# Kernel tuning notes

Measured on AMD Instinct MI355X. Metric: run time of the kernel, lower is better.

Reference implementation:

```python
import jax, jax.numpy as jnp
import numpy as np

B, S, D, UNITS = 8, 2048, 512, 512

def setup_inputs() -> dict:
    key = jax.random.key(0)
    k1, k2, k3, k4 = jax.random.split(key, 4)
    scale = 1.0 / np.sqrt(D)
    return {
        "x": jax.random.normal(k1, (B, S, D), dtype=jnp.float32),
        "Wq": jax.random.normal(k2, (D, UNITS), dtype=jnp.float32) * scale,
        "Wk": jax.random.normal(k3, (D, UNITS), dtype=jnp.float32) * scale,
        "Wv": jax.random.normal(k4, (D, UNITS), dtype=jnp.float32) * scale,
    }

def reference(x, Wq, Wk, Wv):
    # Q, K, V: [B, S, units]
    Q = jnp.einsum('bsd,du->bsu', x, Wq)
    Km = jnp.einsum('bsd,du->bsu', x, Wk)
    V = jnp.einsum('bsd,du->bsu', x, Wv)
    d_k = jnp.asarray(Wq.shape[-1], dtype=x.dtype)
    # scores: [B, S, S]
    scores = jnp.einsum('bqu,bku->bqk', Q, Km) / jnp.sqrt(d_k)
    attn = jax.nn.softmax(scores, axis=-1)
    return jnp.einsum('bqk,bku->bqu', attn, V)
```

## Files before the change

kernel.cpp:

```cpp
#include <hip/hip_runtime.h>

typedef __attribute__((ext_vector_type(8))) __bf16 bf16x8;
typedef __attribute__((ext_vector_type(4))) float f32x4;
typedef unsigned short u16;
typedef unsigned int u32;

#define VMCNT(n) asm volatile("s_waitcnt vmcnt(" #n ")" ::: "memory")
#define LGKMCNT0 asm volatile("s_waitcnt lgkmcnt(0)" ::: "memory")

__device__ __forceinline__ u16 f2bf(float f) {
  union { float f; u32 u; } v; v.f = f;
  u32 r = v.u + 0x7FFFu + ((v.u >> 16) & 1u);
  return (u16)(r >> 16);
}
__device__ __forceinline__ float fexp2(float x) {
  float r; asm("v_exp_f32 %0, %1" : "=v"(r) : "v"(x)); return r;
}

__global__ __launch_bounds__(256) void cast_x_kernel(const float* __restrict__ x,
                                                     u16* __restrict__ xb, int n4) {
  int i = blockIdx.x * 256 + threadIdx.x;
  if (i >= n4) return;
  float4 v = reinterpret_cast<const float4*>(x)[i];
  ushort4 o;
  o.x = f2bf(v.x); o.y = f2bf(v.y); o.z = f2bf(v.z); o.w = f2bf(v.w);
  reinterpret_cast<ushort4*>(xb)[i] = o;
}

__global__ __launch_bounds__(1024) void transpose_w_kernel(const float* __restrict__ Wq,
                                                           const float* __restrict__ Wk,
                                                           const float* __restrict__ Wv,
                                                           u16* __restrict__ Wt) {
  const float* src = blockIdx.z == 0 ? Wq : (blockIdx.z == 1 ? Wk : Wv);
  u16* dst = Wt + (size_t)blockIdx.z * 512 * 512;
  __shared__ float tile[32][33];
  int u0 = blockIdx.x * 32, d0 = blockIdx.y * 32;
  tile[threadIdx.y][threadIdx.x] = src[(d0 + threadIdx.y) * 512 + u0 + threadIdx.x];
  __syncthreads();
  dst[(u0 + threadIdx.y) * 512 + d0 + threadIdx.x] = f2bf(tile[threadIdx.x][threadIdx.y]);
}

__global__ __launch_bounds__(256) void qkv_kernel(const u16* __restrict__ Xb,
                                                  const u16* __restrict__ Wt3,
                                                  u16* __restrict__ Q, u16* __restrict__ K,
                                                  u16* __restrict__ Vt2) {
  __shared__ u16 As[3][128 * 32], Bs[3][128 * 32];
  const int bm = blockIdx.y * 128;
  const int bn = blockIdx.x * 128;
  const int z = blockIdx.z;
  const u16* A = Xb + (size_t)bm * 512;
  const u16* Bt = Wt3 + (size_t)z * 512 * 512 + (size_t)bn * 512;

  const int t = threadIdx.x;
  const int lane = t & 63;
  const int w = t >> 6;
  const int wr = w >> 1, wc = w & 1;
  const int la = lane & 15;
  const int q = lane >> 4;
  f32x4 acc[4][4] = {};

  auto stage = [&](int buf, int kt) {
    const int k0 = kt * 32;
#pragma unroll
    for (int it = 0; it < 2; ++it) {
      int c = it * 256 + t, row = c >> 2;
      int col = ((c & 3) ^ ((row >> 1) & 3)) << 3;
      __builtin_amdgcn_global_load_lds(
          (const __attribute__((address_space(1))) void*)(A + (size_t)row * 512 + k0 + col),
          (__attribute__((address_space(3))) void*)(&As[buf][c * 8]), 16, 0, 0);
    }
#pragma unroll
    for (int it = 0; it < 2; ++it) {
      int c = it * 256 + t, row = c >> 2;
      int col = ((c & 3) ^ ((row >> 1) & 3)) << 3;
      __builtin_amdgcn_global_load_lds(
          (const __attribute__((address_space(1))) void*)(Bt + (size_t)row * 512 + k0 + col),
          (__attribute__((address_space(3))) void*)(&Bs[buf][c * 8]), 16, 0, 0);
    }
  };

  auto body = [&](int buf) {
    bf16x8 a[4], b[4];
#pragma unroll
    for (int i = 0; i < 4; ++i) {
      int row = wr * 64 + i * 16 + la;
      a[i] = *reinterpret_cast<const bf16x8*>(&As[buf][row * 32 + ((q ^ ((row >> 1) & 3)) << 3)]);
    }
#pragma unroll
    for (int j = 0; j < 4; ++j) {
      int row = wc * 64 + j * 16 + la;
      b[j] = *reinterpret_cast<const bf16x8*>(&Bs[buf][row * 32 + ((q ^ ((row >> 1) & 3)) << 3)]);
    }
    __builtin_amdgcn_s_setprio(1);
#pragma unroll
    for (int i = 0; i < 4; ++i)
#pragma unroll
      for (int j = 0; j < 4; ++j)
        acc[i][j] = __builtin_amdgcn_mfma_f32_16x16x32_bf16(a[i], b[j], acc[i][j], 0, 0, 0);
    __builtin_amdgcn_s_setprio(0);
  };

  stage(0, 0); stage(1, 1);
  int cb = 0, sb = 2;
  for (int kt = 0; kt < 14; ++kt) {
    VMCNT(4);
    __builtin_amdgcn_s_barrier();
    stage(sb, kt + 2);
    body(cb);
    cb = (cb == 2) ? 0 : cb + 1;
    sb = (sb == 2) ? 0 : sb + 1;
  }
  VMCNT(4); __builtin_amdgcn_s_barrier(); body(2);
  VMCNT(0); __builtin_amdgcn_s_barrier(); body(0);

  const int r0 = q * 4, cn = lane & 15;
  if (z < 2) {
    u16* out = (z == 0) ? Q : K;
#pragma unroll
    for (int i = 0; i < 4; ++i)
#pragma unroll
      for (int j = 0; j < 4; ++j)
#pragma unroll
        for (int r = 0; r < 4; ++r) {
          int m = bm + 64 * wr + 16 * i + r0 + r;
          int n = bn + 64 * wc + 16 * j + cn;
          out[(size_t)m * 512 + n] = f2bf(acc[i][j][r]);
        }
  } else {
#pragma unroll
    for (int i = 0; i < 4; ++i)
#pragma unroll
      for (int j = 0; j < 4; ++j)
#pragma unroll
        for (int r = 0; r < 4; ++r) {
          int m = bm + 64 * wr + 16 * i + r0 + r;
          int u = bn + 64 * wc + 16 * j + cn;
          int b = m >> 11, s = m & 2047;
          Vt2[(((size_t)b * 64 + (s >> 5)) * 512 + u) * 32 + (s & 31)] = f2bf(acc[i][j][r]);
        }
  }
}

__global__ __launch_bounds__(512) void scores8_kernel(const u16* __restrict__ Q,
                                                      const u16* __restrict__ K,
                                                      u16* __restrict__ S2) {
  __shared__ u16 ring[4][2][256 * 32];
  const int bb = blockIdx.x;
  const int bm = blockIdx.y * 256;
  const int bn = blockIdx.z * 256;
  const u16* Aq = Q + (size_t)(bb * 2048 + bm) * 512;
  const u16* Bk = K + (size_t)(bb * 2048 + bn) * 512;

  const int t = threadIdx.x;
  const int lane = t & 63;
  const int wid = t >> 6;
  const int wm = wid >> 2, wn = wid & 3;
  const int la = lane & 15;
  const int q = lane >> 4;

  f32x4 acc[8][4] = {};

  auto stage = [&](int kt) {
    const int r = kt & 3;
    const int koff = kt * 32;
#pragma unroll
    for (int half = 0; half < 2; ++half) {
      int c = half * 512 + t;
      int row = c >> 2;
      int col = ((c & 3) ^ ((row >> 1) & 3)) << 3;
      __builtin_amdgcn_global_load_lds(
          (const __attribute__((address_space(1))) void*)(Aq + (size_t)row * 512 + koff + col),
          (__attribute__((address_space(3))) void*)(&ring[r][0][c * 8]), 16, 0, 0);
      __builtin_amdgcn_global_load_lds(
          (const __attribute__((address_space(1))) void*)(Bk + (size_t)row * 512 + koff + col),
          (__attribute__((address_space(3))) void*)(&ring[r][1][c * 8]), 16, 0, 0);
    }
  };

  auto body = [&](int kt) {
    const int r = kt & 3;
    const u16* At = ring[r][0];
    const u16* Bt = ring[r][1];
    bf16x8 bfr[4], afr[8];
#pragma unroll
    for (int j = 0; j < 4; ++j) {
      int row = wn * 64 + j * 16 + la;
      bfr[j] = *reinterpret_cast<const bf16x8*>(Bt + row * 32 + ((q ^ ((row >> 1) & 3)) << 3));
    }
#pragma unroll
    for (int i = 0; i < 8; ++i) {
      int row = wm * 128 + i * 16 + la;
      afr[i] = *reinterpret_cast<const bf16x8*>(At + row * 32 + ((q ^ ((row >> 1) & 3)) << 3));
    }
    __builtin_amdgcn_s_setprio(1);
#pragma unroll
    for (int i = 0; i < 8; ++i)
#pragma unroll
      for (int j = 0; j < 4; ++j)
        acc[i][j] = __builtin_amdgcn_mfma_f32_16x16x32_bf16(afr[i], bfr[j], acc[i][j], 0, 0, 0);
    __builtin_amdgcn_s_setprio(0);
  };

  stage(0); stage(1); stage(2);
  for (int kt = 0; kt < 13; ++kt) {
    VMCNT(8);
    __builtin_amdgcn_s_barrier();
    stage(kt + 3);
    body(kt);
  }
  VMCNT(8); __builtin_amdgcn_s_barrier(); body(13);
  VMCNT(4); __builtin_amdgcn_s_barrier(); body(14);
  VMCNT(0); __builtin_amdgcn_s_barrier(); body(15);

  const float scale = 0.06375872127f;
  const int r0h = q * 4;
#pragma unroll
  for (int i = 0; i < 8; ++i)
#pragma unroll
    for (int j = 0; j < 4; ++j) {
      int n = bn + wn * 64 + j * 16;
      int kt_j = n >> 5;
      int ke_j = (n & 31) + la;
      u16* dst = S2 + ((size_t)(bb * 64 + kt_j) * 2048) * 32 + ke_j;
#pragma unroll
      for (int r = 0; r < 4; ++r) {
        int m = bm + wm * 128 + i * 16 + r0h + r;
        dst[(size_t)m * 32] = f2bf(fexp2(acc[i][j][r] * scale));
      }
    }
}

__global__ __launch_bounds__(512, 4) void pv_kernel(const u16* __restrict__ S2,
                                                    const u16* __restrict__ Vt2,
                                                    float* __restrict__ out) {
  __shared__ __align__(16) char smem[65536];
  __shared__ float larr2[2][128];
  u16* As = (u16*)smem;
  u16* Bs = As + 2 * 8192;
  float* scratch = (float*)smem;

  const int id = blockIdx.x;
  const int b = id & 7;
  const int local = id >> 3;
  const int bn = (local & 3) * 128;
  const int bm = (local >> 2) * 128;

  const u16* A2 = S2 + ((size_t)b * 64 * 2048 + (size_t)bm) * 32;
  const u16* B2 = Vt2 + ((size_t)b * 64 * 512 + (size_t)bn) * 32;

  const int t = threadIdx.x;
  const int lane = t & 63;
  const int wid = t >> 6;
  const int wm = (wid >> 2) & 1;
  const int wn = (wid >> 1) & 1;
  const int wk = wid & 1;
  const int la = lane & 15;
  const int q = lane >> 4;

  f32x4 acc[4][4] = {};
  float lacc[4] = {0.f, 0.f, 0.f, 0.f};

  auto stage = [&](int s) {
    const int buf = s & 1;
#pragma unroll
    for (int it = 0; it < 2; ++it) {
      int c = it * 512 + t;
      int row = c >> 3, pslot = c & 7;
      int lslot = pslot ^ (row & 7);
      __builtin_amdgcn_global_load_lds(
          (const __attribute__((address_space(1))) void*)(
              A2 + (size_t)(2 * s + (lslot >> 2)) * 65536 + row * 32 + (lslot & 3) * 8),
          (__attribute__((address_space(3))) void*)(As + buf * 8192 + c * 8), 16, 0, 0);
    }
#pragma unroll
    for (int it = 0; it < 2; ++it) {
      int c = it * 512 + t;
      int row = c >> 3, pslot = c & 7;
      int lslot = pslot ^ (row & 7);
      __builtin_amdgcn_global_load_lds(
          (const __attribute__((address_space(1))) void*)(
              B2 + (size_t)(2 * s + (lslot >> 2)) * 16384 + row * 32 + (lslot & 3) * 8),
          (__attribute__((address_space(3))) void*)(Bs + buf * 8192 + c * 8), 16, 0, 0);
    }
  };

  bf16x8 a[4], bb[4];
  auto rd = [&](int buf) {
    const u16* Ab = As + buf * 8192;
    const u16* Bb = Bs + buf * 8192;
#pragma unroll
    for (int i = 0; i < 4; ++i) {
      int row = wm * 64 + i * 16 + la;
      int ps = (wk * 4 + q) ^ (row & 7);
      a[i] = *reinterpret_cast<const bf16x8*>(Ab + row * 64 + ps * 8);
    }
#pragma unroll
    for (int j = 0; j < 4; ++j) {
      int row = wn * 64 + j * 16 + la;
      int ps = (wk * 4 + q) ^ (row & 7);
      bb[j] = *reinterpret_cast<const bf16x8*>(Bb + row * 64 + ps * 8);
    }
  };
  auto compute = [&]() {
    if (wn == 0) {
#pragma unroll
      for (int i = 0; i < 4; ++i) {
        float ls = 0.f;
#pragma unroll
        for (int e = 0; e < 8; ++e) ls += (float)a[i][e];
        lacc[i] += ls;
      }
    }
    __builtin_amdgcn_s_setprio(1);
#pragma unroll
    for (int i = 0; i < 4; ++i)
#pragma unroll
      for (int j = 0; j < 4; ++j)
        acc[i][j] = __builtin_amdgcn_mfma_f32_16x16x32_bf16(a[i], bb[j], acc[i][j], 0, 0, 0);
    __builtin_amdgcn_s_setprio(0);
  };

  stage(0); stage(1);
  for (int s = 0; s < 30; ++s) {
    VMCNT(4);
    __builtin_amdgcn_s_barrier();
    rd(s & 1);
    LGKMCNT0;
    __builtin_amdgcn_s_barrier();
    stage(s + 2);
    compute();
  }
  VMCNT(4); __builtin_amdgcn_s_barrier();
  rd(0); LGKMCNT0; __builtin_amdgcn_s_barrier(); compute();
  VMCNT(0); __builtin_amdgcn_s_barrier();
  rd(1); LGKMCNT0; __builtin_amdgcn_s_barrier();
  compute();

  float l[4];
#pragma unroll
  for (int i = 0; i < 4; ++i) {
    l[i] = lacc[i];
    l[i] += __shfl_xor(l[i], 16);
    l[i] += __shfl_xor(l[i], 32);
  }
  if (wn == 0 && q == 0) {
#pragma unroll
    for (int i = 0; i < 4; ++i) larr2[wk][wm * 64 + i * 16 + la] = l[i];
  }
  float* sp = scratch + (wid >> 1) * 4096;
  if (wk == 1) {
#pragma unroll
    for (int i = 0; i < 4; ++i)
#pragma unroll
      for (int j = 0; j < 4; ++j)
        *reinterpret_cast<f32x4*>(sp + (i * 4 + j) * 256 + lane * 4) = acc[i][j];
  }
  __syncthreads();
  if (wk == 0) {
#pragma unroll
    for (int i = 0; i < 4; ++i)
#pragma unroll
      for (int j = 0; j < 4; ++j) {
        f32x4 o = *reinterpret_cast<const f32x4*>(sp + (i * 4 + j) * 256 + lane * 4);
#pragma unroll
        for (int r = 0; r < 4; ++r) acc[i][j][r] += o[r];
      }
    float* C = out + ((size_t)b * 2048 + bm) * 512;
    const int r0 = q * 4, cn = lane & 15;
    float inv[4][4];
#pragma unroll
    for (int i = 0; i < 4; ++i)
#pragma unroll
      for (int r = 0; r < 4; ++r) {
        int row = wm * 64 + i * 16 + r0 + r;
        inv[i][r] = 1.0f / (larr2[0][row] + larr2[1][row]);
      }
#pragma unroll
    for (int i = 0; i < 4; ++i)
#pragma unroll
      for (int j = 0; j < 4; ++j)
#pragma unroll
        for (int r = 0; r < 4; ++r) {
          int m = wm * 64 + 16 * i + r0 + r;
          int n = bn + 64 * wn + 16 * j + cn;
          C[(size_t)m * 512 + n] = acc[i][j][r] * inv[i][r];
        }
  }
}

extern "C" void kernel_launch(void* const* d_in, const int* in_sizes, int n_in,
                              void* d_out, int out_size, void* d_ws, size_t ws_size,
                              hipStream_t stream) {
  const float* x  = (const float*)d_in[0];
  const float* Wq = (const float*)d_in[1];
  const float* Wk = (const float*)d_in[2];
  const float* Wv = (const float*)d_in[3];
  float* out = (float*)d_out;

  char* p = (char*)d_ws;
  u16* Xb = (u16*)p;            p += (size_t)16384 * 512 * 2;
  u16* Wt = (u16*)p;            p += (size_t)3 * 512 * 512 * 2;
  u16* Q  = (u16*)p;            p += (size_t)16384 * 512 * 2;
  u16* K  = (u16*)p;            p += (size_t)16384 * 512 * 2;
  u16* Vt2 = (u16*)p;           p += (size_t)16384 * 512 * 2;
  u16* S2 = (u16*)p;

  cast_x_kernel<<<dim3(8192), dim3(256), 0, stream>>>(x, Xb, 16384 * 512 / 4);
  transpose_w_kernel<<<dim3(16, 16, 3), dim3(32, 32), 0, stream>>>(Wq, Wk, Wv, Wt);
  qkv_kernel<<<dim3(4, 128, 3), dim3(256), 0, stream>>>(Xb, Wt, Q, K, Vt2);
  scores8_kernel<<<dim3(8, 8, 8), dim3(512), 0, stream>>>(Q, K, S2);
  pv_kernel<<<dim3(512), dim3(512), 0, stream>>>(S2, Vt2, out);
}
```

Before: 140.2 us.

## Load PV A-operand directly to registers and triple-buffer B in LDS

In the PV kernel, each wave now loads its slice of the probability matrix straight from global memory into double-buffered registers, instead of staging it through LDS. Only the V tile still goes through LDS, which moves from two buffers to three. The loop is unrolled by two and uses one barrier per step instead of two. This removes LDS traffic and a barrier for A, at the cost of more registers and uncoalesced direct global loads. There is also a risk of race conditions with the three-buffer scheme and the vmcnt accounting.

After: 183.8 us. 1.31x slower.

```diff
diff --git a/kernel.cpp b/kernel.cpp
--- a/kernel.cpp
+++ b/kernel.cpp
@@ -235,8 +235,7 @@
                                                     float* __restrict__ out) {
   __shared__ __align__(16) char smem[65536];
   __shared__ float larr2[2][128];
-  u16* As = (u16*)smem;
-  u16* Bs = As + 2 * 8192;
+  u16* Bs = (u16*)smem;
   float* scratch = (float*)smem;
 
   const int id = blockIdx.x;
@@ -260,18 +259,17 @@
   f32x4 acc[4][4] = {};
   float lacc[4] = {0.f, 0.f, 0.f, 0.f};
 
-  auto stage = [&](int s) {
-    const int buf = s & 1;
-#pragma unroll
-    for (int it = 0; it < 2; ++it) {
-      int c = it * 512 + t;
-      int row = c >> 3, pslot = c & 7;
-      int lslot = pslot ^ (row & 7);
-      __builtin_amdgcn_global_load_lds(
-          (const __attribute__((address_space(1))) void*)(
-              A2 + (size_t)(2 * s + (lslot >> 2)) * 65536 + row * 32 + (lslot & 3) * 8),
-          (__attribute__((address_space(3))) void*)(As + buf * 8192 + c * 8), 16, 0, 0);
-    }
+  const u16* aPtr = A2 + (size_t)wk * 65536 + (size_t)(wm * 64 + la) * 32 + q * 8;
+
+  auto loadA = [&](bf16x8 (&dst)[4]) {
+#pragma unroll
+    for (int i = 0; i < 4; ++i)
+      dst[i] = *reinterpret_cast<const bf16x8*>(aPtr + i * 512);
+    aPtr += 131072;
+  };
+
+  auto stageB = [&](int s) {
+    const int buf = s % 3;
 #pragma unroll
     for (int it = 0; it < 2; ++it) {
       int c = it * 512 + t;
@@ -284,16 +282,9 @@
     }
   };
 
-  bf16x8 a[4], bb[4];
-  auto rd = [&](int buf) {
-    const u16* Ab = As + buf * 8192;
-    const u16* Bb = Bs + buf * 8192;
-#pragma unroll
-    for (int i = 0; i < 4; ++i) {
-      int row = wm * 64 + i * 16 + la;
-      int ps = (wk * 4 + q) ^ (row & 7);
-      a[i] = *reinterpret_cast<const bf16x8*>(Ab + row * 64 + ps * 8);
-    }
+  bf16x8 aA[4], aB[4], bb[4];
+  auto rdB = [&](int s) {
+    const u16* Bb = Bs + (s % 3) * 8192;
 #pragma unroll
     for (int j = 0; j < 4; ++j) {
       int row = wn * 64 + j * 16 + la;
@@ -301,7 +292,7 @@
       bb[j] = *reinterpret_cast<const bf16x8*>(Bb + row * 64 + ps * 8);
     }
   };
-  auto compute = [&]() {
+  auto compute = [&](bf16x8 (&a)[4]) {
     if (wn == 0) {
 #pragma unroll
       for (int i = 0; i < 4; ++i) {
@@ -320,21 +311,27 @@
     __builtin_amdgcn_s_setprio(0);
   };
 
-  stage(0); stage(1);
-  for (int s = 0; s < 30; ++s) {
-    VMCNT(4);
-    __builtin_amdgcn_s_barrier();
-    rd(s & 1);
-    LGKMCNT0;
-    __builtin_amdgcn_s_barrier();
-    stage(s + 2);
-    compute();
-  }
-  VMCNT(4); __builtin_amdgcn_s_barrier();
-  rd(0); LGKMCNT0; __builtin_amdgcn_s_barrier(); compute();
+  loadA(aA);
+  stageB(0); stageB(1);
+  VMCNT(2);
+  __builtin_amdgcn_s_barrier();
+
+  for (int s = 0; s < 30; s += 2) {
+    loadA(aB); stageB(s + 2);
+    rdB(s);
+    compute(aA);
+    VMCNT(2); __builtin_amdgcn_s_barrier();
+    loadA(aA); stageB(s + 3);
+    rdB(s + 1);
+    compute(aB);
+    VMCNT(2); __builtin_amdgcn_s_barrier();
+  }
+  loadA(aB);
+  rdB(30);
+  compute(aA);
   VMCNT(0); __builtin_amdgcn_s_barrier();
-  rd(1); LGKMCNT0; __builtin_amdgcn_s_barrier();
-  compute();
+  rdB(31); LGKMCNT0; __builtin_amdgcn_s_barrier();
+  compute(aB);
 
   float l[4];
 #pragma unroll
```

## Shrink scores tile to 256x128 with 3-stage ring and batch-interleaved grid

Applied to the files above, without the earlier changes.

The scores GEMM moves from 256x256 tiles with a 4-deep LDS ring to 256x128 tiles with a 3-deep ring. It launches as a 1D grid of 1024 blocks with the batch index in the low bits, and the launch bounds are set to target 4 blocks per CU. The aim is more blocks, higher occupancy and better spreading of work across CUs. In exchange each tile reuses less data, so K traffic per FLOP rises, and the shallower prefetch pipeline hides less load latency.

Result: no change. 142.8 us (median of 2 runs) (+1.9%).

```diff
diff --git a/kernel.cpp b/kernel.cpp
--- a/kernel.cpp
+++ b/kernel.cpp
@@ -141,90 +141,95 @@
   }
 }
 
-__global__ __launch_bounds__(512) void scores8_kernel(const u16* __restrict__ Q,
-                                                      const u16* __restrict__ K,
-                                                      u16* __restrict__ S2) {
-  __shared__ u16 ring[4][2][256 * 32];
-  const int bb = blockIdx.x;
-  const int bm = blockIdx.y * 256;
-  const int bn = blockIdx.z * 256;
-  const u16* Aq = Q + (size_t)(bb * 2048 + bm) * 512;
-  const u16* Bk = K + (size_t)(bb * 2048 + bn) * 512;
+__global__ __launch_bounds__(512, 4) void scores_kernel(const u16* __restrict__ Q,
+                                                        const u16* __restrict__ K,
+                                                        u16* __restrict__ S2) {
+  __shared__ u16 As[3][256 * 32], Bs[3][128 * 32];
+  const int id = blockIdx.x;
+  const int b = id & 7;
+  const int local = id >> 3;
+  const int qi = local & 7;
+  const int ki = local >> 3;
+  const int bm = qi * 256;
+  const int bn = ki * 128;
+  const u16* Aq = Q + (size_t)(b * 2048 + bm) * 512;
+  const u16* Bk = K + (size_t)(b * 2048 + bn) * 512;
 
   const int t = threadIdx.x;
   const int lane = t & 63;
   const int wid = t >> 6;
-  const int wm = wid >> 2, wn = wid & 3;
+  const int wm = wid >> 1;
+  const int wn = wid & 1;
   const int la = lane & 15;
   const int q = lane >> 4;
 
-  f32x4 acc[8][4] = {};
+  f32x4 acc[4][4] = {};
 
   auto stage = [&](int kt) {
-    const int r = kt & 3;
+    const int buf = kt % 3;
     const int koff = kt * 32;
 #pragma unroll
-    for (int half = 0; half < 2; ++half) {
-      int c = half * 512 + t;
-      int row = c >> 2;
+    for (int it = 0; it < 2; ++it) {
+      int c = it * 512 + t, row = c >> 2;
       int col = ((c & 3) ^ ((row >> 1) & 3)) << 3;
       __builtin_amdgcn_global_load_lds(
           (const __attribute__((address_space(1))) void*)(Aq + (size_t)row * 512 + koff + col),
-          (__attribute__((address_space(3))) void*)(&ring[r][0][c * 8]), 16, 0, 0);
+          (__attribute__((address_space(3))) void*)(&As[buf][c * 8]), 16, 0, 0);
+    }
+    {
+      int c = t, row = c >> 2;
+      int col = ((c & 3) ^ ((row >> 1) & 3)) << 3;
       __builtin_amdgcn_global_load_lds(
           (const __attribute__((address_space(1))) void*)(Bk + (size_t)row * 512 + koff + col),
-          (__attribute__((address_space(3))) void*)(&ring[r][1][c * 8]), 16, 0, 0);
+          (__attribute__((address_space(3))) void*)(&Bs[buf][c * 8]), 16, 0, 0);
     }
   };
 
   auto body = [&](int kt) {
-    const int r = kt & 3;
-    const u16* At = ring[r][0];
-    const u16* Bt = ring[r][1];
-    bf16x8 bfr[4], afr[8];
+    const int buf = kt % 3;
+    bf16x8 a[4], bb[4];
+#pragma unroll
+    for (int i = 0; i < 4; ++i) {
+      int row = wm * 64 + i * 16 + la;
+      a[i] = *reinterpret_cast<const bf16x8*>(&As[buf][row * 32 + ((q ^ ((row >> 1) & 3)) << 3)]);
+    }
 #pragma unroll
     for (int j = 0; j < 4; ++j) {
       int row = wn * 64 + j * 16 + la;
-      bfr[j] = *reinterpret_cast<const bf16x8*>(Bt + row * 32 + ((q ^ ((row >> 1) & 3)) << 3));
-    }
-#pragma unroll
-    for (int i = 0; i < 8; ++i) {
-      int row = wm * 128 + i * 16 + la;
-      afr[i] = *reinterpret_cast<const bf16x8*>(At + row * 32 + ((q ^ ((row >> 1) & 3)) << 3));
+      bb[j] = *reinterpret_cast<const bf16x8*>(&Bs[buf][row * 32 + ((q ^ ((row >> 1) & 3)) << 3)]);
     }
     __builtin_amdgcn_s_setprio(1);
 #pragma unroll
-    for (int i = 0; i < 8; ++i)
-#pragma unroll
-      for (int j = 0; j < 4; ++j)
-        acc[i][j] = __builtin_amdgcn_mfma_f32_16x16x32_bf16(afr[i], bfr[j], acc[i][j], 0, 0, 0);
+    for (int i = 0; i < 4; ++i)
+#pragma unroll
+      for (int j = 0; j < 4; ++j)
+        acc[i][j] = __builtin_amdgcn_mfma_f32_16x16x32_bf16(a[i], bb[j], acc[i][j], 0, 0, 0);
     __builtin_amdgcn_s_setprio(0);
   };
 
-  stage(0); stage(1); stage(2);
-  for (int kt = 0; kt < 13; ++kt) {
-    VMCNT(8);
+  stage(0); stage(1);
+  for (int kt = 0; kt < 14; ++kt) {
+    VMCNT(3);
     __builtin_amdgcn_s_barrier();
-    stage(kt + 3);
+    stage(kt + 2);
     body(kt);
   }
-  VMCNT(8); __builtin_amdgcn_s_barrier(); body(13);
-  VMCNT(4); __builtin_amdgcn_s_barrier(); body(14);
+  VMCNT(3); __builtin_amdgcn_s_barrier(); body(14);
   VMCNT(0); __builtin_amdgcn_s_barrier(); body(15);
 
   const float scale = 0.06375872127f;
   const int r0h = q * 4;
 #pragma unroll
-  for (int i = 0; i < 8; ++i)
+  for (int i = 0; i < 4; ++i)
 #pragma unroll
     for (int j = 0; j < 4; ++j) {
       int n = bn + wn * 64 + j * 16;
       int kt_j = n >> 5;
       int ke_j = (n & 31) + la;
-      u16* dst = S2 + ((size_t)(bb * 64 + kt_j) * 2048) * 32 + ke_j;
+      u16* dst = S2 + ((size_t)(b * 64 + kt_j) * 2048) * 32 + ke_j;
 #pragma unroll
       for (int r = 0; r < 4; ++r) {
-        int m = bm + wm * 128 + i * 16 + r0h + r;
+        int m = bm + wm * 64 + i * 16 + r0h + r;
         dst[(size_t)m * 32] = f2bf(fexp2(acc[i][j][r] * scale));
       }
     }
@@ -408,6 +413,6 @@
   cast_x_kernel<<<dim3(8192), dim3(256), 0, stream>>>(x, Xb, 16384 * 512 / 4);
   transpose_w_kernel<<<dim3(16, 16, 3), dim3(32, 32), 0, stream>>>(Wq, Wk, Wv, Wt);
   qkv_kernel<<<dim3(4, 128, 3), dim3(256), 0, stream>>>(Xb, Wt, Q, K, Vt2);
-  scores8_kernel<<<dim3(8, 8, 8), dim3(512), 0, stream>>>(Q, K, S2);
+  scores_kernel<<<dim3(1024), dim3(512), 0, stream>>>(Q, K, S2);
   pv_kernel<<<dim3(512), dim3(512), 0, stream>>>(S2, Vt2, out);
 }
```
